# Performance work log

Measured on AMD Instinct MI355X. Metric: run time of the kernel, lower is better.

Reference implementation:

```python
import jax, jax.numpy as jnp
import numpy as np

FS, STRIDE, PAD = 3, 1, 1

def setup_inputs() -> dict:
    key = jax.random.key(0)
    k1, k2, k3 = jax.random.split(key, 3)
    N, C, H, W = 4, 256, 64, 64
    out_C = 256
    x = jax.random.normal(k1, (N, C, H, W), jnp.float32)
    # offset/mask conv params (original inits to 0 -> degenerate; use small random)
    offset_w = jax.random.normal(k2, (FS * FS * 3, C, FS, FS), jnp.float32) * 0.01
    offset_b = jnp.zeros((FS * FS * 3,), jnp.float32)
    # xavier_normal-like scale for dcn weight
    dcn_w = jax.random.normal(k3, (out_C, C, FS, FS), jnp.float32) * (1.0 / np.sqrt(C * FS * FS))
    return {"x": x, "offset_w": offset_w, "offset_b": offset_b, "dcn_w": dcn_w}

def _dcnv2(x, offset_w, offset_b, dcn_w):
    fs, stride, pad = FS, STRIDE, PAD
    N, C, H, W = x.shape
    out_C = dcn_w.shape[0]
    K2 = fs * fs
    om = jax.lax.conv_general_dilated(
        x, offset_w, (stride, stride), [(pad, pad), (pad, pad)],
        dimension_numbers=("NCHW", "OIHW", "NCHW")) + offset_b[None, :, None, None]
    Ho, Wo = om.shape[2], om.shape[3]
    offset = om[:, : 2 * K2].reshape(N, K2, 2, Ho, Wo)
    off_y, off_x = offset[:, :, 0], offset[:, :, 1]            # [N,K2,Ho,Wo]
    mask = jax.nn.sigmoid(om[:, 2 * K2:])                      # [N,K2,Ho,Wo]
    # base sampling grid: ori + kernel tap offset
    ky, kx = jnp.meshgrid(jnp.arange(fs), jnp.arange(fs), indexing="ij")
    ky = ky.reshape(K2).astype(jnp.float32)
    kx = kx.reshape(K2).astype(jnp.float32)
    base_y = (jnp.arange(Ho, dtype=jnp.float32) * stride - pad)[None, :, None] + ky[:, None, None]
    base_x = (jnp.arange(Wo, dtype=jnp.float32) * stride - pad)[None, None, :] + kx[:, None, None]
    h_im = base_y[None] + off_y                                # [N,K2,Ho,Wo]
    w_im = base_x[None] + off_x
    y0 = jnp.floor(h_im)
    x0 = jnp.floor(w_im)
    lh, lw = h_im - y0, w_im - x0
    xf = x.reshape(N, C, H * W)

    def gather(yi, xi):
        valid = (yi >= 0) & (yi <= H - 1) & (xi >= 0) & (xi <= W - 1)
        yc = jnp.clip(yi, 0, H - 1).astype(jnp.int32)
        xc = jnp.clip(xi, 0, W - 1).astype(jnp.int32)
        idx = (yc * W + xc).reshape(N, -1)
        v = jax.vmap(lambda img, ind: img[:, ind])(xf, idx)    # [N,C,K2*Ho*Wo]
        v = v.reshape(N, C, K2, Ho, Wo)
        return v * valid[:, None].astype(x.dtype)

    hh, hw = 1.0 - lh, 1.0 - lw
    sampled = ((hh * hw)[:, None] * gather(y0, x0)
               + (hh * lw)[:, None] * gather(y0, x0 + 1)
               + (lh * hw)[:, None] * gather(y0 + 1, x0)
               + (lh * lw)[:, None] * gather(y0 + 1, x0 + 1))  # [N,C,K2,Ho,Wo]
    sampled = sampled * mask[:, None]
    wk = dcn_w.reshape(out_C, C, K2)
    return jnp.einsum("nckhw,ock->nohw", sampled, wk)

def reference(x, offset_w, offset_b, dcn_w):
    return _dcnv2(x, offset_w, offset_b, dcn_w)
```

## Files before the change

kernel.cpp:

```cpp
#include <hip/hip_runtime.h>
#include <hip/hip_bf16.h>
#include <math.h>

#define NB     4
#define CIN    256
#define HH     64
#define WW     64
#define OUTC   256
#define K2     9
#define KTOT   2304
#define HWSZ   4096
#define NSTEPS 72
#define MTOT   16384


typedef __attribute__((ext_vector_type(4)))  float  floatx4;
typedef __attribute__((ext_vector_type(16))) float  floatx16;
typedef __attribute__((ext_vector_type(8)))  short  short8;
typedef __attribute__((ext_vector_type(4)))  short  short4v;
typedef __attribute__((ext_vector_type(4)))  int    intx4;

__device__ __forceinline__ unsigned short f2bf(float f) {
  union { float f; unsigned u; } v; v.f = f;
  unsigned r = v.u + 0x7FFF + ((v.u >> 16) & 1);
  return (unsigned short)(r >> 16);
}
__device__ __forceinline__ float b2f(unsigned short s) {
  union { unsigned u; float f; } v; v.u = ((unsigned)s) << 16;
  return v.f;
}

#define WSM_BFRAG   0
#define WSM_B2FRAG  1179648
#define WSM_XT      (1179648 + 147456)
#define WSM_END     (WSM_XT + NB * HWSZ * CIN * 2)
#define WSF_BW      0
#define WSF_B2W     (KTOT * OUTC * 2)
#define WSF_OM      (WSF_B2W + KTOT * 32 * 2)
#define WSF_END     (WSF_OM + NB * 27 * HWSZ * 4)

__global__ __launch_bounds__(256) void prep_main_kernel(
    const float* __restrict__ dcn_w, const float* __restrict__ offw,
    const float* __restrict__ x,
    unsigned short* __restrict__ Bfrag, unsigned short* __restrict__ B2frag,
    unsigned short* __restrict__ xt) {
  int bid = blockIdx.x;
  int tid = threadIdx.x;
  if (bid < 256) {
    __shared__ unsigned short T[64 * 266];
    int img = bid >> 6, h = bid & 63;
    const float* xp = x + (size_t)img * CIN * HWSZ + h * 64;
    int w = tid & 63, cq = tid >> 6;
    for (int cb = 0; cb < 256; cb += 4) {
      int c = cb + cq;
      T[w * 266 + c] = f2bf(xp[(size_t)c * HWSZ + w]);
    }
    __syncthreads();
    int w2 = tid >> 2, cg = (tid & 3) << 6;
    unsigned short* o = xt + ((size_t)(img * 64 + h) * 64 + w2) * 256 + cg;
#pragma unroll
    for (int i = 0; i < 64; i += 8) {
      short8 v = *(short8*)&T[w2 * 266 + cg + i];
      *(short8*)(o + i) = v;
    }
  } else if (bid < 544) {
    int e = (bid - 256) * 256 + tid;
    int lane = e & 63, nt = (e >> 6) & 7, s16 = e >> 9;
    int n = nt * 32 + (lane & 31);
    int kb = s16 * 16 + ((lane >> 5) << 3);
    short8 pk;
#pragma unroll
    for (int j = 0; j < 8; ++j) {
      int k = kb + j;
      pk[j] = (short)f2bf(dcn_w[n * KTOT + (k & 255) * 9 + (k >> 8)]);
    }
    *(short8*)(Bfrag + (size_t)e * 8) = pk;
  } else {
    int e = (bid - 544) * 256 + tid;
    int lane = e & 63, nt = (e >> 6) & 1, s32 = e >> 7;
    int n = nt * 16 + (lane & 15);
    int kb = s32 * 32 + ((lane >> 4) << 3);
    short8 pk;
#pragma unroll
    for (int j = 0; j < 8; ++j) {
      int k = kb + j;
      pk[j] = (n < 27) ? (short)f2bf(offw[n * KTOT + (k & 255) * 9 + (k >> 8)])
                       : (short)0;
    }
    *(short8*)(B2frag + (size_t)e * 8) = pk;
  }
}

__global__ __launch_bounds__(256, 1) void dcn_fused_kernel(
    const unsigned short* __restrict__ xt,
    const unsigned short* __restrict__ Bfrag,
    const unsigned short* __restrict__ B2frag,
    const float* __restrict__ ob, float* __restrict__ out) {
  __shared__ unsigned short Ald[2][8][64][8];
  __shared__ intx4  sOff[576];
  __shared__ float4 sWt[576];
  __shared__ float  omp[4 * 32 * 68];

  int bid = blockIdx.x;
  int img = bid >> 6, h = bid & 63;
  const unsigned short* xb = xt + (size_t)img * HWSZ * 256;

  int tid  = threadIdx.x;
  int lane = tid & 63, q = tid >> 6;
  int quad = lane >> 4, l15 = lane & 15;
  int l31  = lane & 31,  lh = lane >> 5;

  {
    floatx4 cacc[4][2];
#pragma unroll
    for (int mt = 0; mt < 4; ++mt)
#pragma unroll
      for (int nt = 0; nt < 2; ++nt) cacc[mt][nt] = (floatx4){0.f, 0.f, 0.f, 0.f};
    short8 cpa[2][4];
    short8 cpb[2][2];

#define CONV_LOAD(I, SLOT)                                                     \
  {                                                                            \
    int s = q + (I) * 4;                                                       \
    int t = s >> 3;                                                            \
    int dy = t / 3 - 1, dx = t % 3 - 1;                                        \
    int y = h + dy;                                                            \
    int cb0 = ((s & 7) << 5) + (quad << 3);                                    \
    _Pragma("unroll")                                                          \
    for (int mt = 0; mt < 4; ++mt) {                                           \
      int xx = mt * 16 + l15 + dx;                                             \
      short8 v = {0, 0, 0, 0, 0, 0, 0, 0};                                     \
      if (((unsigned)y < 64u) && ((unsigned)xx < 64u))                         \
        v = *(const short8*)(xb + ((y * 64 + xx) << 8) + cb0);                 \
      cpa[SLOT][mt] = v;                                                       \
    }                                                                          \
    _Pragma("unroll")                                                          \
    for (int nt = 0; nt < 2; ++nt)                                             \
      cpb[SLOT][nt] = *(const short8*)(B2frag + (((s * 2 + nt) * 64 + lane) << 3)); \
  }

    CONV_LOAD(0, 0);
#pragma unroll 2
    for (int i = 0; i < 18; ++i) {
      int sl = i & 1;
      if (i < 17) CONV_LOAD(i + 1, sl ^ 1);
#pragma unroll
      for (int mt = 0; mt < 4; ++mt)
#pragma unroll
        for (int nt = 0; nt < 2; ++nt)
          cacc[mt][nt] = __builtin_amdgcn_mfma_f32_16x16x32_bf16(
              cpa[sl][mt], cpb[sl][nt], cacc[mt][nt], 0, 0, 0);
    }
#undef CONV_LOAD
#pragma unroll
    for (int mt = 0; mt < 4; ++mt)
#pragma unroll
      for (int nt = 0; nt < 2; ++nt) {
        int oc = nt * 16 + l15;
        float4 vv = make_float4(cacc[mt][nt][0], cacc[mt][nt][1],
                                cacc[mt][nt][2], cacc[mt][nt][3]);
        *(float4*)&omp[(q * 32 + oc) * 68 + mt * 16 + quad * 4] = vv;
      }
  }
  __syncthreads();

  for (int v = tid; v < 576; v += 256) {
    int w = v & 63, t = v >> 6;
    int ky = t / 3, kx = t % 3;
    float offy = omp[(0 * 32 + 2 * t) * 68 + w] + omp[(1 * 32 + 2 * t) * 68 + w] +
                 omp[(2 * 32 + 2 * t) * 68 + w] + omp[(3 * 32 + 2 * t) * 68 + w] +
                 ob[2 * t];
    float offx = omp[(0 * 32 + 2 * t + 1) * 68 + w] + omp[(1 * 32 + 2 * t + 1) * 68 + w] +
                 omp[(2 * 32 + 2 * t + 1) * 68 + w] + omp[(3 * 32 + 2 * t + 1) * 68 + w] +
                 ob[2 * t + 1];
    float mraw = omp[(0 * 32 + 18 + t) * 68 + w] + omp[(1 * 32 + 18 + t) * 68 + w] +
                 omp[(2 * 32 + 18 + t) * 68 + w] + omp[(3 * 32 + 18 + t) * 68 + w] +
                 ob[18 + t];
    float mv   = 1.0f / (1.0f + __expf(-mraw));
    float him  = (float)(h - 1 + ky) + offy;
    float wim  = (float)(w - 1 + kx) + offx;
    float y0f = floorf(him), x0f = floorf(wim);
    float lhf = him - y0f, lwf = wim - x0f;
    int y0 = (int)y0f, x0i = (int)x0f;
    bool vy0 = (y0 >= 0) && (y0 < HH);
    bool vy1 = (y0 + 1 >= 0) && (y0 + 1 < HH);
    bool vx0 = (x0i >= 0) && (x0i < WW);
    bool vx1 = (x0i + 1 >= 0) && (x0i + 1 < WW);
    float hh_ = 1.0f - lhf, hw_ = 1.0f - lwf;
    float4 wt;
    wt.x = (vy0 && vx0) ? hh_ * hw_ * mv : 0.0f;
    wt.y = (vy0 && vx1) ? hh_ * lwf * mv : 0.0f;
    wt.z = (vy1 && vx0) ? lhf * hw_ * mv : 0.0f;
    wt.w = (vy1 && vx1) ? lhf * lwf * mv : 0.0f;
    int y0c = min(max(y0, 0), 63), y1c = min(max(y0 + 1, 0), 63);
    int x0c = min(max(x0i, 0), 63), x1c = min(max(x0i + 1, 0), 63);
    intx4 ii = {(y0c * 64 + x0c) << 8, (y0c * 64 + x1c) << 8,
                (y1c * 64 + x0c) << 8, (y1c * 64 + x1c) << 8};
    sOff[v] = ii;
    sWt[v]  = wt;
  }
  __syncthreads();

  floatx16 acc[2][2];
#pragma unroll
  for (int mt = 0; mt < 2; ++mt)
#pragma unroll
    for (int nt = 0; nt < 2; ++nt)
#pragma unroll
      for (int e = 0; e < 16; ++e) acc[mt][nt][e] = 0.f;

  int m   = tid >> 2;
  int ch0 = tid & 3;
  int mtm = m >> 5, m31 = m & 31;

  short8 bfr[2][8];
  short8 cr[2][4];
  float4 pwt;

#pragma unroll
  for (int sub = 0; sub < 4; ++sub)
#pragma unroll
    for (int nt = 0; nt < 2; ++nt)
      bfr[0][sub * 2 + nt] = *(const short8*)(
          Bfrag + (((size_t)sub * 8 + (q * 2 + nt)) * 64 + lane) * 8);
  {
    intx4 off = sOff[m];
    pwt = sWt[m];
    int cb = ch0 * 8;
#pragma unroll
    for (int sl = 0; sl < 2; ++sl) {
      int cc = cb + sl * 32;
      cr[sl][0] = *(const short8*)(xb + off.x + cc);
      cr[sl][1] = *(const short8*)(xb + off.y + cc);
      cr[sl][2] = *(const short8*)(xb + off.z + cc);
      cr[sl][3] = *(const short8*)(xb + off.w + cc);
    }
  }
#pragma unroll
  for (int sl = 0; sl < 2; ++sl) {
    int ch = ch0 + sl * 4;
    short8 pk;
#pragma unroll
    for (int j = 0; j < 8; ++j) {
      float v = pwt.x * b2f((unsigned short)cr[sl][0][j]) +
                pwt.y * b2f((unsigned short)cr[sl][1][j]) +
                pwt.z * b2f((unsigned short)cr[sl][2][j]) +
                pwt.w * b2f((unsigned short)cr[sl][3][j]);
      pk[j] = (short)f2bf(v);
    }
    *(short8*)&Ald[0][(ch >> 1) * 2 + mtm][(ch & 1) * 32 + m31][0] = pk;
  }
  {
    intx4 off = sOff[m];
    pwt = sWt[m];
    int cb = 64 + ch0 * 8;
#pragma unroll
    for (int sl = 0; sl < 2; ++sl) {
      int cc = cb + sl * 32;
      cr[sl][0] = *(const short8*)(xb + off.x + cc);
      cr[sl][1] = *(const short8*)(xb + off.y + cc);
      cr[sl][2] = *(const short8*)(xb + off.z + cc);
      cr[sl][3] = *(const short8*)(xb + off.w + cc);
    }
  }
  __syncthreads();

#pragma unroll 2
  for (int s = 0; s < 36; ++s) {
    int cur = s & 1;
    if (s < 35) {
      int s16b = (s + 1) * 4;
#pragma unroll
      for (int sub = 0; sub < 4; ++sub)
#pragma unroll
        for (int nt = 0; nt < 2; ++nt)
          bfr[cur ^ 1][sub * 2 + nt] = *(const short8*)(
              Bfrag + (((size_t)(s16b + sub) * 8 + (q * 2 + nt)) * 64 + lane) * 8);
    }
    if (s < 35) {
#pragma unroll
      for (int sl = 0; sl < 2; ++sl) {
        int ch = ch0 + sl * 4;
        short8 pk;
#pragma unroll
        for (int j = 0; j < 8; ++j) {
          float v = pwt.x * b2f((unsigned short)cr[sl][0][j]) +
                    pwt.y * b2f((unsigned short)cr[sl][1][j]) +
                    pwt.z * b2f((unsigned short)cr[sl][2][j]) +
                    pwt.w * b2f((unsigned short)cr[sl][3][j]);
          pk[j] = (short)f2bf(v);
        }
        *(short8*)&Ald[cur ^ 1][(ch >> 1) * 2 + mtm][(ch & 1) * 32 + m31][0] = pk;
      }
    }
    if (s < 34) {
      int s2 = s + 2;
      int t2 = s2 >> 2;
      intx4 off = sOff[t2 * 64 + m];
      pwt = sWt[t2 * 64 + m];
      int cb = (s2 & 3) * 64 + ch0 * 8;
#pragma unroll
      for (int sl = 0; sl < 2; ++sl) {
        int cc = cb + sl * 32;
        cr[sl][0] = *(const short8*)(xb + off.x + cc);
        cr[sl][1] = *(const short8*)(xb + off.y + cc);
        cr[sl][2] = *(const short8*)(xb + off.z + cc);
        cr[sl][3] = *(const short8*)(xb + off.w + cc);
      }
    }
#pragma unroll
    for (int sub = 0; sub < 4; ++sub) {
      short8 a0 = *(short8*)&Ald[cur][sub * 2 + 0][lane][0];
      short8 a1 = *(short8*)&Ald[cur][sub * 2 + 1][lane][0];
#pragma unroll
      for (int nt = 0; nt < 2; ++nt) {
        acc[0][nt] = __builtin_amdgcn_mfma_f32_32x32x16_bf16(
            a0, bfr[cur][sub * 2 + nt], acc[0][nt], 0, 0, 0);
        acc[1][nt] = __builtin_amdgcn_mfma_f32_32x32x16_bf16(
            a1, bfr[cur][sub * 2 + nt], acc[1][nt], 0, 0, 0);
      }
    }
    __syncthreads();
  }

#pragma unroll
  for (int mt = 0; mt < 2; ++mt)
#pragma unroll
    for (int nt = 0; nt < 2; ++nt) {
      int oc = q * 64 + nt * 32 + l31;
      float* obase = out + (((size_t)img * OUTC + oc) << 12) + h * 64 +
                     mt * 32 + lh * 4;
#pragma unroll
      for (int rg = 0; rg < 4; ++rg) {
        float4 vv = make_float4(acc[mt][nt][rg * 4 + 0], acc[mt][nt][rg * 4 + 1],
                                acc[mt][nt][rg * 4 + 2], acc[mt][nt][rg * 4 + 3]);
        *(float4*)(obase + rg * 8) = vv;
      }
    }
}

__global__ __launch_bounds__(256) void prep_fb_kernel(
    const float* __restrict__ dcn_w, const float* __restrict__ offw,
    unsigned short* __restrict__ Bw, unsigned short* __restrict__ B2w) {
  int oc = blockIdx.x;
  for (int k = threadIdx.x; k < KTOT; k += 256) {
    int t = k >> 8, c = k & 255;
    Bw[oc * KTOT + k] = f2bf(dcn_w[oc * KTOT + c * 9 + t]);
    if (oc < 32)
      B2w[oc * KTOT + k] = (oc < 27) ? f2bf(offw[oc * KTOT + c * 9 + t])
                                     : (unsigned short)0;
  }
}

__global__ __launch_bounds__(256) void conv_offset_kernel(
    const float* __restrict__ x, const unsigned short* __restrict__ B2w,
    const float* __restrict__ ob, float* __restrict__ om) {
  __shared__ unsigned short A_lds[64 * 40];
  __shared__ unsigned short B_lds[32 * 40];
  int bid = blockIdx.x;
  int n = bid >> 6, h = bid & 63;
  int tid = threadIdx.x, lane = tid & 63, q = tid >> 6;
  const float* xn = x + n * (CIN * HWSZ);
  floatx4 acc0 = {0.f, 0.f, 0.f, 0.f}, acc1 = {0.f, 0.f, 0.f, 0.f};
  int w = tid & 63, cg = tid >> 6, ocb = tid >> 3, part = tid & 7;
  for (int s = 0; s < NSTEPS; ++s) {
    int t = s >> 3, c0 = (s & 7) << 5;
    int dy = t / 3 - 1, dx = t % 3 - 1;
    __syncthreads();
    {
      int y = h + dy, xx = w + dx;
      bool inb = ((unsigned)y < 64u) && ((unsigned)xx < 64u);
      const float* xb = xn + (c0 + cg * 8) * HWSZ + y * 64 + xx;
      short8 pk;
#pragma unroll
      for (int j = 0; j < 8; ++j) { float v = inb ? xb[j * HWSZ] : 0.0f; pk[j] = (short)f2bf(v); }
      *(short8*)&A_lds[w * 40 + cg * 8] = pk;
    }
    { const unsigned short* bp = B2w + ocb * KTOT + (t << 8) + c0 + part * 4;
      *(short4v*)&B_lds[ocb * 40 + part * 4] = *(const short4v*)bp; }
    __syncthreads();
    int fr = (lane >> 4) * 8;
    short8 af  = *(short8*)&A_lds[(q * 16 + (lane & 15)) * 40 + fr];
    short8 bf0 = *(short8*)&B_lds[((lane & 15)) * 40 + fr];
    short8 bf1 = *(short8*)&B_lds[(16 + (lane & 15)) * 40 + fr];
    acc0 = __builtin_amdgcn_mfma_f32_16x16x32_bf16(af, bf0, acc0, 0, 0, 0);
    acc1 = __builtin_amdgcn_mfma_f32_16x16x32_bf16(af, bf1, acc1, 0, 0, 0);
  }
  int g = lane >> 4;
#pragma unroll
  for (int nt = 0; nt < 2; ++nt) {
    floatx4 a = nt ? acc1 : acc0;
    int oc = nt * 16 + (lane & 15);
    if (oc < 27) {
      float bias = ob[oc];
#pragma unroll
      for (int r = 0; r < 4; ++r) {
        int wm = q * 16 + g * 4 + r;
        float val = a[r] + bias;
        if (oc >= 18) val = 1.0f / (1.0f + __expf(-val));
        om[((n * 27 + oc) << 12) + h * 64 + wm] = val;
      }
    }
  }
}

__global__ __launch_bounds__(256) void dcn_main_kernel(
    const float* __restrict__ x, const float* __restrict__ om,
    const unsigned short* __restrict__ Bw, float* __restrict__ out) {
  __shared__ unsigned short A_lds[32 * 40];
  __shared__ unsigned short B_lds[256 * 40];
  __shared__ int    sY[288];
  __shared__ int    sX[288];
  __shared__ float4 sW[288];
  int bid = blockIdx.x;
  int n = bid >> 7, rem = bid & 127, h = rem >> 1, w0 = (rem & 1) << 5;
  int tid = threadIdx.x, lane = tid & 63, q = tid >> 6;
  const float* xn  = x + n * (CIN * HWSZ);
  const float* omn = om + n * (27 * HWSZ);
  for (int v = tid; v < 288; v += 256) {
    int m = v & 31, t = v >> 5;
    int ky = t / 3, kx = t % 3;
    int wg = w0 + m, sp = h * 64 + wg;
    float offy = omn[(2 * t) * HWSZ + sp];
    float offx = omn[(2 * t + 1) * HWSZ + sp];
    float mv   = omn[(18 + t) * HWSZ + sp];
    float him = (float)(h - 1 + ky) + offy;
    float wim = (float)(wg - 1 + kx) + offx;
    float y0f = floorf(him), x0f = floorf(wim);
    float lh = him - y0f, lw = wim - x0f;
    int y0 = (int)y0f, x0i = (int)x0f;
    bool vy0 = (y0 >= 0) && (y0 < HH), vy1 = (y0 + 1 >= 0) && (y0 + 1 < HH);
    bool vx0 = (x0i >= 0) && (x0i < WW), vx1 = (x0i + 1 >= 0) && (x0i + 1 < WW);
    float hh_ = 1.0f - lh, hw_ = 1.0f - lw;
    float4 wt;
    wt.x = (vy0 && vx0) ? hh_ * hw_ * mv : 0.0f;
    wt.y = (vy0 && vx1) ? hh_ * lw  * mv : 0.0f;
    wt.z = (vy1 && vx0) ? lh  * hw_ * mv : 0.0f;
    wt.w = (vy1 && vx1) ? lh  * lw  * mv : 0.0f;
    sY[v] = y0; sX[v] = x0i; sW[v] = wt;
  }
  floatx4 acc[2][4];
#pragma unroll
  for (int mi = 0; mi < 2; ++mi)
#pragma unroll
    for (int nj = 0; nj < 4; ++nj) acc[mi][nj] = (floatx4){0.f, 0.f, 0.f, 0.f};
  int m = tid & 31, cg = tid >> 5, n0 = q * 64;
  for (int s = 0; s < NSTEPS; ++s) {
    int t = s >> 3, c0 = (s & 7) << 5;
    __syncthreads();
    {
      int p = t * 32 + m;
      int y0 = sY[p], x0i = sX[p];
      float4 wt = sW[p];
      int y0c = min(max(y0, 0), 63), y1c = min(max(y0 + 1, 0), 63);
      int x0c = min(max(x0i, 0), 63), x1c = min(max(x0i + 1, 0), 63);
      int i00 = y0c * 64 + x0c, i01 = y0c * 64 + x1c;
      int i10 = y1c * 64 + x0c, i11 = y1c * 64 + x1c;
      const float* xb = xn + (c0 + cg * 4) * HWSZ;
      short4v pk;
#pragma unroll
      for (int j = 0; j < 4; ++j) {
        const float* xc = xb + j * HWSZ;
        float v = wt.x * xc[i00] + wt.y * xc[i01] + wt.z * xc[i10] + wt.w * xc[i11];
        pk[j] = (short)f2bf(v);
      }
      *(short4v*)&A_lds[m * 40 + cg * 4] = pk;
    }
    {
      const short8* bp = (const short8*)(Bw + tid * KTOT + (t << 8) + c0);
      short8 b0 = bp[0], b1 = bp[1], b2 = bp[2], b3 = bp[3];
      short8* dst = (short8*)&B_lds[tid * 40];
      dst[0] = b0; dst[1] = b1; dst[2] = b2; dst[3] = b3;
    }
    __syncthreads();
    int fr = (lane >> 4) * 8;
    short8 a0 = *(short8*)&A_lds[((lane & 15)) * 40 + fr];
    short8 a1 = *(short8*)&A_lds[(16 + (lane & 15)) * 40 + fr];
#pragma unroll
    for (int nj = 0; nj < 4; ++nj) {
      short8 bfp = *(short8*)&B_lds[(n0 + nj * 16 + (lane & 15)) * 40 + fr];
      acc[0][nj] = __builtin_amdgcn_mfma_f32_16x16x32_bf16(a0, bfp, acc[0][nj], 0, 0, 0);
      acc[1][nj] = __builtin_amdgcn_mfma_f32_16x16x32_bf16(a1, bfp, acc[1][nj], 0, 0, 0);
    }
  }
  int g = lane >> 4;
#pragma unroll
  for (int mi = 0; mi < 2; ++mi) {
    int wm = w0 + mi * 16 + g * 4;
#pragma unroll
    for (int nj = 0; nj < 4; ++nj) {
      int oc = n0 + nj * 16 + (lane & 15);
      float4 vv = make_float4(acc[mi][nj][0], acc[mi][nj][1],
                              acc[mi][nj][2], acc[mi][nj][3]);
      *(float4*)&out[((n * OUTC + oc) << 12) + h * 64 + wm] = vv;
    }
  }
}

extern "C" void kernel_launch(void* const* d_in, const int* in_sizes, int n_in,
                              void* d_out, int out_size, void* d_ws, size_t ws_size,
                              hipStream_t stream) {
  const float* x     = (const float*)d_in[0];
  const float* offw  = (const float*)d_in[1];
  const float* ob    = (const float*)d_in[2];
  const float* dcn_w = (const float*)d_in[3];
  float* out = (float*)d_out;

  if (ws_size >= (size_t)WSM_END) {
    unsigned short* Bfrag  = (unsigned short*)((char*)d_ws + WSM_BFRAG);
    unsigned short* B2frag = (unsigned short*)((char*)d_ws + WSM_B2FRAG);
    unsigned short* xtb    = (unsigned short*)((char*)d_ws + WSM_XT);
    prep_main_kernel<<<580, 256, 0, stream>>>(dcn_w, offw, x, Bfrag, B2frag, xtb);
    dcn_fused_kernel<<<256, 256, 0, stream>>>(xtb, Bfrag, B2frag, ob, out);
  } else {
    unsigned short* Bw  = (unsigned short*)((char*)d_ws + WSF_BW);
    unsigned short* B2w = (unsigned short*)((char*)d_ws + WSF_B2W);
    float*          omb = (float*)((char*)d_ws + WSF_OM);
    prep_fb_kernel<<<256, 256, 0, stream>>>(dcn_w, offw, Bw, B2w);
    conv_offset_kernel<<<NB * HH, 256, 0, stream>>>(x, B2w, ob, omb);
    dcn_main_kernel<<<NB * HH * 2, 256, 0, stream>>>(x, omb, Bw, out);
  }
}
```

Before: 134.9 us.

## Double fused DCN block to 512 threads and pad LDS A-tile layout

```diff
diff --git a/kernel.cpp b/kernel.cpp
--- a/kernel.cpp
+++ b/kernel.cpp
@@ -91,12 +91,12 @@
   }
 }
 
-__global__ __launch_bounds__(256, 1) void dcn_fused_kernel(
+__global__ __launch_bounds__(512, 2) void dcn_fused_kernel(
     const unsigned short* __restrict__ xt,
     const unsigned short* __restrict__ Bfrag,
     const unsigned short* __restrict__ B2frag,
     const float* __restrict__ ob, float* __restrict__ out) {
-  __shared__ unsigned short Ald[2][8][64][8];
+  __shared__ unsigned short Ald[2][520 * 8];
   __shared__ intx4  sOff[576];
   __shared__ float4 sWt[576];
   __shared__ float  omp[4 * 32 * 68];
@@ -108,9 +108,9 @@
   int tid  = threadIdx.x;
   int lane = tid & 63, q = tid >> 6;
   int quad = lane >> 4, l15 = lane & 15;
-  int l31  = lane & 31,  lh = lane >> 5;
-
-  {
+  int l31  = lane & 31,  lh5 = lane >> 5;
+
+  if (q < 4) {
     floatx4 cacc[4][2];
 #pragma unroll
     for (int mt = 0; mt < 4; ++mt)
@@ -164,7 +164,7 @@
   }
   __syncthreads();
 
-  for (int v = tid; v < 576; v += 256) {
+  for (int v = tid; v < 576; v += 512) {
     int w = v & 63, t = v >> 6;
     int ky = t / 3, kx = t % 3;
     float offy = omp[(0 * 32 + 2 * t) * 68 + w] + omp[(1 * 32 + 2 * t) * 68 + w] +
@@ -199,69 +199,54 @@
     sOff[v] = ii;
     sWt[v]  = wt;
   }
+
+  floatx16 acc[2];
+#pragma unroll
+  for (int mt = 0; mt < 2; ++mt)
+#pragma unroll
+    for (int e = 0; e < 16; ++e) acc[mt][e] = 0.f;
+
+  int sm  = tid >> 3;
+  int chk = tid & 7;
+  int wgran = (((chk >> 1) << 1) + (sm >> 5)) * 65 + ((chk & 1) << 5) + (sm & 31);
+
+  short8 bfr[2][4];
+  short8 cr[4];
+  float4 pwt;
+
   __syncthreads();
 
-  floatx16 acc[2][2];
-#pragma unroll
-  for (int mt = 0; mt < 2; ++mt)
-#pragma unroll
-    for (int nt = 0; nt < 2; ++nt)
-#pragma unroll
-      for (int e = 0; e < 16; ++e) acc[mt][nt][e] = 0.f;
-
-  int m   = tid >> 2;
-  int ch0 = tid & 3;
-  int mtm = m >> 5, m31 = m & 31;
-
-  short8 bfr[2][8];
-  short8 cr[2][4];
-  float4 pwt;
-
 #pragma unroll
   for (int sub = 0; sub < 4; ++sub)
-#pragma unroll
-    for (int nt = 0; nt < 2; ++nt)
-      bfr[0][sub * 2 + nt] = *(const short8*)(
-          Bfrag + (((size_t)sub * 8 + (q * 2 + nt)) * 64 + lane) * 8);
+    bfr[0][sub] = *(const short8*)(
+        Bfrag + (((size_t)sub * 8 + q) * 64 + lane) * 8);
   {
-    intx4 off = sOff[m];
-    pwt = sWt[m];
-    int cb = ch0 * 8;
-#pragma unroll
-    for (int sl = 0; sl < 2; ++sl) {
-      int cc = cb + sl * 32;
-      cr[sl][0] = *(const short8*)(xb + off.x + cc);
-      cr[sl][1] = *(const short8*)(xb + off.y + cc);
-      cr[sl][2] = *(const short8*)(xb + off.z + cc);
-      cr[sl][3] = *(const short8*)(xb + off.w + cc);
-    }
-  }
-#pragma unroll
-  for (int sl = 0; sl < 2; ++sl) {
-    int ch = ch0 + sl * 4;
+    intx4 off = sOff[sm];
+    float4 w0 = sWt[sm];
+    int cb = chk * 8;
+    cr[0] = *(const short8*)(xb + off.x + cb);
+    cr[1] = *(const short8*)(xb + off.y + cb);
+    cr[2] = *(const short8*)(xb + off.z + cb);
+    cr[3] = *(const short8*)(xb + off.w + cb);
     short8 pk;
 #pragma unroll
     for (int j = 0; j < 8; ++j) {
-      float v = pwt.x * b2f((unsigned short)cr[sl][0][j]) +
-                pwt.y * b2f((unsigned short)cr[sl][1][j]) +
-                pwt.z * b2f((unsigned short)cr[sl][2][j]) +
-                pwt.w * b2f((unsigned short)cr[sl][3][j]);
+      float v = w0.x * b2f((unsigned short)cr[0][j]) +
+                w0.y * b2f((unsigned short)cr[1][j]) +
+                w0.z * b2f((unsigned short)cr[2][j]) +
+                w0.w * b2f((unsigned short)cr[3][j]);
       pk[j] = (short)f2bf(v);
     }
-    *(short8*)&Ald[0][(ch >> 1) * 2 + mtm][(ch & 1) * 32 + m31][0] = pk;
+    *(short8*)&Ald[0][wgran * 8] = pk;
   }
   {
-    intx4 off = sOff[m];
-    pwt = sWt[m];
-    int cb = 64 + ch0 * 8;
-#pragma unroll
-    for (int sl = 0; sl < 2; ++sl) {
-      int cc = cb + sl * 32;
-      cr[sl][0] = *(const short8*)(xb + off.x + cc);
-      cr[sl][1] = *(const short8*)(xb + off.y + cc);
-      cr[sl][2] = *(const short8*)(xb + off.z + cc);
-      cr[sl][3] = *(const short8*)(xb + off.w + cc);
-    }
+    intx4 off = sOff[sm];
+    pwt = sWt[sm];
+    int cb = 64 + chk * 8;
+    cr[0] = *(const short8*)(xb + off.x + cb);
+    cr[1] = *(const short8*)(xb + off.y + cb);
+    cr[2] = *(const short8*)(xb + off.z + cb);
+    cr[3] = *(const short8*)(xb + off.w + cb);
   }
   __syncthreads();
 
@@ -272,71 +257,54 @@
       int s16b = (s + 1) * 4;
 #pragma unroll
       for (int sub = 0; sub < 4; ++sub)
-#pragma unroll
-        for (int nt = 0; nt < 2; ++nt)
-          bfr[cur ^ 1][sub * 2 + nt] = *(const short8*)(
-              Bfrag + (((size_t)(s16b + sub) * 8 + (q * 2 + nt)) * 64 + lane) * 8);
-    }
-    if (s < 35) {
-#pragma unroll
-      for (int sl = 0; sl < 2; ++sl) {
-        int ch = ch0 + sl * 4;
-        short8 pk;
-#pragma unroll
-        for (int j = 0; j < 8; ++j) {
-          float v = pwt.x * b2f((unsigned short)cr[sl][0][j]) +
-                    pwt.y * b2f((unsigned short)cr[sl][1][j]) +
-                    pwt.z * b2f((unsigned short)cr[sl][2][j]) +
-                    pwt.w * b2f((unsigned short)cr[sl][3][j]);
-          pk[j] = (short)f2bf(v);
-        }
-        *(short8*)&Ald[cur ^ 1][(ch >> 1) * 2 + mtm][(ch & 1) * 32 + m31][0] = pk;
+        bfr[cur ^ 1][sub] = *(const short8*)(
+            Bfrag + (((size_t)(s16b + sub) * 8 + q) * 64 + lane) * 8);
+      short8 pk;
+#pragma unroll
+      for (int j = 0; j < 8; ++j) {
+        float v = pwt.x * b2f((unsigned short)cr[0][j]) +
+                  pwt.y * b2f((unsigned short)cr[1][j]) +
+                  pwt.z * b2f((unsigned short)cr[2][j]) +
+                  pwt.w * b2f((unsigned short)cr[3][j]);
+        pk[j] = (short)f2bf(v);
       }
+      *(short8*)&Ald[cur ^ 1][wgran * 8] = pk;
     }
     if (s < 34) {
       int s2 = s + 2;
       int t2 = s2 >> 2;
-      intx4 off = sOff[t2 * 64 + m];
-      pwt = sWt[t2 * 64 + m];
-      int cb = (s2 & 3) * 64 + ch0 * 8;
-#pragma unroll
-      for (int sl = 0; sl < 2; ++sl) {
-        int cc = cb + sl * 32;
-        cr[sl][0] = *(const short8*)(xb + off.x + cc);
-        cr[sl][1] = *(const short8*)(xb + off.y + cc);
-        cr[sl][2] = *(const short8*)(xb + off.z + cc);
-        cr[sl][3] = *(const short8*)(xb + off.w + cc);
-      }
+      intx4 off = sOff[t2 * 64 + sm];
+      pwt = sWt[t2 * 64 + sm];
+      int cb = (s2 & 3) * 64 + chk * 8;
+      cr[0] = *(const short8*)(xb + off.x + cb);
+      cr[1] = *(const short8*)(xb + off.y + cb);
+      cr[2] = *(const short8*)(xb + off.z + cb);
+      cr[3] = *(const short8*)(xb + off.w + cb);
     }
 #pragma unroll
     for (int sub = 0; sub < 4; ++sub) {
-      short8 a0 = *(short8*)&Ald[cur][sub * 2 + 0][lane][0];
-      short8 a1 = *(short8*)&Ald[cur][sub * 2 + 1][lane][0];
-#pragma unroll
-      for (int nt = 0; nt < 2; ++nt) {
-        acc[0][nt] = __builtin_amdgcn_mfma_f32_32x32x16_bf16(
-            a0, bfr[cur][sub * 2 + nt], acc[0][nt], 0, 0, 0);
-        acc[1][nt] = __builtin_amdgcn_mfma_f32_32x32x16_bf16(
-            a1, bfr[cur][sub * 2 + nt], acc[1][nt], 0, 0, 0);
-      }
-    }
-    __syncthreads();
-  }
-
-#pragma unroll
-  for (int mt = 0; mt < 2; ++mt)
-#pragma unroll
-    for (int nt = 0; nt < 2; ++nt) {
-      int oc = q * 64 + nt * 32 + l31;
-      float* obase = out + (((size_t)img * OUTC + oc) << 12) + h * 64 +
-                     mt * 32 + lh * 4;
-#pragma unroll
-      for (int rg = 0; rg < 4; ++rg) {
-        float4 vv = make_float4(acc[mt][nt][rg * 4 + 0], acc[mt][nt][rg * 4 + 1],
-                                acc[mt][nt][rg * 4 + 2], acc[mt][nt][rg * 4 + 3]);
-        *(float4*)(obase + rg * 8) = vv;
-      }
-    }
+      short8 a0 = *(short8*)&Ald[cur][((sub * 2 + 0) * 65 + lane) * 8];
+      short8 a1 = *(short8*)&Ald[cur][((sub * 2 + 1) * 65 + lane) * 8];
+      acc[0] = __builtin_amdgcn_mfma_f32_32x32x16_bf16(
+          a0, bfr[cur][sub], acc[0], 0, 0, 0);
+      acc[1] = __builtin_amdgcn_mfma_f32_32x32x16_bf16(
+          a1, bfr[cur][sub], acc[1], 0, 0, 0);
+    }
+    __syncthreads();
+  }
+
+  int oc = q * 32 + l31;
+#pragma unroll
+  for (int mt = 0; mt < 2; ++mt) {
+    float* obase = out + (((size_t)img * OUTC + oc) << 12) + h * 64 +
+                   mt * 32 + lh5 * 4;
+#pragma unroll
+    for (int rg = 0; rg < 4; ++rg) {
+      float4 vv = make_float4(acc[mt][rg * 4 + 0], acc[mt][rg * 4 + 1],
+                              acc[mt][rg * 4 + 2], acc[mt][rg * 4 + 3]);
+      *(float4*)(obase + rg * 8) = vv;
+    }
+  }
 }
 
 __global__ __launch_bounds__(256) void prep_fb_kernel(
@@ -511,7 +479,7 @@
     unsigned short* B2frag = (unsigned short*)((char*)d_ws + WSM_B2FRAG);
     unsigned short* xtb    = (unsigned short*)((char*)d_ws + WSM_XT);
     prep_main_kernel<<<580, 256, 0, stream>>>(dcn_w, offw, x, Bfrag, B2frag, xtb);
-    dcn_fused_kernel<<<256, 256, 0, stream>>>(xtb, Bfrag, B2frag, ob, out);
+    dcn_fused_kernel<<<256, 512, 0, stream>>>(xtb, Bfrag, B2frag, ob, out);
   } else {
     unsigned short* Bw  = (unsigned short*)((char*)d_ws + WSF_BW);
     unsigned short* B2w = (unsigned short*)((char*)d_ws + WSF_B2W);
```

Result: faster. 127.1 us (-5.8%).
